# Performance work log

Measured on AMD Instinct MI355X. Metric: run time of the kernel, lower is better.

Reference implementation:

```python
import jax, jax.numpy as jnp
import numpy as np
import math

B, S, D, H = 2, 2048, 2048, 16
HD = D // H  # head_dim = 128
NEG = -9e15


def setup_inputs() -> dict:
    key = jax.random.key(0)
    k1, k2, k3 = jax.random.split(key, 3)
    x = jax.random.normal(k1, (B, S, D), dtype=jnp.float32)
    Wqkv = jax.random.normal(k2, (D, 3 * D), dtype=jnp.float32) * (1.0 / math.sqrt(D))
    bqkv = jnp.zeros((3 * D,), dtype=jnp.float32)
    Wo = jax.random.normal(k3, (D, D), dtype=jnp.float32) * (1.0 / math.sqrt(D))
    bo = jnp.zeros((D,), dtype=jnp.float32)
    return {"x": x, "Wqkv": Wqkv, "bqkv": bqkv, "Wo": Wo, "bo": bo}


def reference(x, Wqkv, bqkv, Wo, bo):
    b, s, d = x.shape
    # fused QKV projection
    qkv = x @ Wqkv + bqkv                       # [B,S,3D]
    qkv = qkv.reshape(b, s, H, 3 * HD)          # per-head interleaved q|k|v
    qkv = qkv.transpose(0, 2, 1, 3)             # [B,H,S,3*HD]
    q, k, v = jnp.split(qkv, 3, axis=-1)        # each [B,H,S,HD]
    scale = 1.0 / math.sqrt(HD)
    logits = jnp.einsum('bhqd,bhkd->bhqk', q, k) * scale  # [B,H,S,S]
    causal = jnp.tril(jnp.ones((s, s), dtype=bool))[None, None]
    logits = jnp.where(causal, logits, NEG)
    score = jax.nn.softmax(logits, axis=-1)
    attn = jnp.einsum('bhqk,bhkd->bhqd', score, v)         # [B,H,S,HD]
    attn = attn.transpose(0, 2, 1, 3).reshape(b, s, d)
    return attn @ Wo + bo
```

## Files before the change

kernel.cpp:

```cpp
#include <hip/hip_runtime.h>
#include <stdint.h>

#define DEV static __device__ __forceinline__

typedef _Float16 half8 __attribute__((ext_vector_type(8)));
typedef float f32x4 __attribute__((ext_vector_type(4)));

constexpr int Bc = 2, Sc = 2048, Dc = 2048, Hc = 16, HDc = 128;
constexpr int D3c = 3 * Dc;
constexpr int Mc = Bc * Sc;

DEV void gl_lds16(const void* g, void* l) {
    __builtin_amdgcn_global_load_lds(
        (const __attribute__((address_space(1))) unsigned int*)g,
        (__attribute__((address_space(3))) unsigned int*)l,
        16, 0, 0);
}

__global__ __launch_bounds__(256) void cast_f16_kernel(
    const float* __restrict__ in, _Float16* __restrict__ out)
{
    int i = blockIdx.x * 256 + threadIdx.x;
    const float4* p = (const float4*)in;
    float4 a = p[i * 2], b = p[i * 2 + 1];
    half8 hv;
    hv[0] = (_Float16)a.x; hv[1] = (_Float16)a.y; hv[2] = (_Float16)a.z; hv[3] = (_Float16)a.w;
    hv[4] = (_Float16)b.x; hv[5] = (_Float16)b.y; hv[6] = (_Float16)b.z; hv[7] = (_Float16)b.w;
    *(half8*)(out + (size_t)i * 8) = hv;
}

__global__ __launch_bounds__(256) void transpose_cast_kernel(
    const float* __restrict__ in, _Float16* __restrict__ out, int R, int C)
{
    __shared__ float ls[64][65];
    const int t = threadIdx.x;
    const int r0 = blockIdx.y * 64, c0 = blockIdx.x * 64;
    const int rr = t >> 6, cc = t & 63;
#pragma unroll
    for (int i = 0; i < 16; ++i) {
        int r = i * 4 + rr;
        ls[r][cc] = in[(size_t)(r0 + r) * C + c0 + cc];
    }
    __syncthreads();
#pragma unroll
    for (int i = 0; i < 16; ++i) {
        int r = i * 4 + rr;
        out[(size_t)(c0 + r) * R + r0 + cc] = (_Float16)ls[cc][r];
    }
}

__global__ __launch_bounds__(256) void transpose_v_kernel(
    const uint16_t* __restrict__ qkv, uint16_t* __restrict__ vt)
{
    __shared__ uint32_t ls[64][65];
    const int t = threadIdx.x;
    const int s0 = blockIdx.x * 64, d0 = blockIdx.y * 64, bh = blockIdx.z;
    const int b = bh >> 4, h = bh & 15;
    const int rr = t >> 6, cc = t & 63;
#pragma unroll
    for (int i = 0; i < 16; ++i) {
        int r = i * 4 + rr;
        ls[r][cc] = qkv[(size_t)(b * Sc + s0 + r) * D3c + h * 384 + 256 + d0 + cc];
    }
    __syncthreads();
#pragma unroll
    for (int i = 0; i < 16; ++i) {
        int r = i * 4 + rr;
        vt[(size_t)(bh * HDc + d0 + r) * Sc + s0 + cc] = (uint16_t)ls[cc][r];
    }
}

template <int BF16OUT>
__global__ __launch_bounds__(256, 2) void gemm_bt_kernel(
    const _Float16* __restrict__ A, const _Float16* __restrict__ Bt,
    const float* __restrict__ bias, void* __restrict__ Cout,
    int M, int N, int K)
{
    __shared__ __align__(16) char smem[32768];
    char* sA = smem;
    char* sB = smem + 16384;
    const int t = threadIdx.x, w = t >> 6, lane = t & 63;
    const int quad = lane >> 4, l15 = lane & 15;
    const int wr = w >> 1, wc = w & 1;
    const int n0 = blockIdx.x * 128, m0 = blockIdx.y * 128;

    const f32x4 vzero = {0.f, 0.f, 0.f, 0.f};
    f32x4 acc[4][4];
#pragma unroll
    for (int i = 0; i < 4; ++i)
#pragma unroll
        for (int j = 0; j < 4; ++j) acc[i][j] = vzero;

    const int kiters = K >> 6;
    for (int kk = 0; kk < kiters; ++kk) {
#pragma unroll
        for (int i = 0; i < 4; ++i) {
            int c = i * 256 + t;
            int row = c >> 3, kbs = c & 7, kact = kbs ^ (row & 7);
            gl_lds16(A + (size_t)(m0 + row) * K + kk * 64 + kact * 8,
                     sA + (i * 256 + w * 64) * 16);
        }
#pragma unroll
        for (int i = 0; i < 4; ++i) {
            int c = i * 256 + t;
            int row = c >> 3, kbs = c & 7, kact = kbs ^ (row & 7);
            gl_lds16(Bt + (size_t)(n0 + row) * K + kk * 64 + kact * 8,
                     sB + (i * 256 + w * 64) * 16);
        }
        __syncthreads();
#pragma unroll
        for (int ks = 0; ks < 2; ++ks) {
            half8 af[4], bf[4];
#pragma unroll
            for (int mt = 0; mt < 4; ++mt) {
                int row = wr * 64 + mt * 16 + l15;
                int kact = (ks * 4 + quad) ^ (l15 & 7);
                af[mt] = *(const half8*)(sA + row * 128 + kact * 16);
            }
#pragma unroll
            for (int nt = 0; nt < 4; ++nt) {
                int row = wc * 64 + nt * 16 + l15;
                int kact = (ks * 4 + quad) ^ (l15 & 7);
                bf[nt] = *(const half8*)(sB + row * 128 + kact * 16);
            }
#pragma unroll
            for (int mt = 0; mt < 4; ++mt)
#pragma unroll
                for (int nt = 0; nt < 4; ++nt)
                    acc[mt][nt] = __builtin_amdgcn_mfma_f32_16x16x32_f16(
                        af[mt], bf[nt], acc[mt][nt], 0, 0, 0);
        }
        __syncthreads();
    }

#pragma unroll
    for (int nt = 0; nt < 4; ++nt) {
        int col = n0 + wc * 64 + nt * 16 + l15;
        float bv = bias[col];
#pragma unroll
        for (int mt = 0; mt < 4; ++mt)
#pragma unroll
            for (int r = 0; r < 4; ++r) {
                int row = m0 + wr * 64 + mt * 16 + quad * 4 + r;
                float v = acc[mt][nt][r] + bv;
                if (BF16OUT) ((_Float16*)Cout)[(size_t)row * N + col] = (_Float16)v;
                else         ((float*)Cout)[(size_t)row * N + col] = v;
            }
    }
}

__global__ __launch_bounds__(256, 2) void flash_kernel(
    const _Float16* __restrict__ qkv, const _Float16* __restrict__ vt,
    _Float16* __restrict__ attn)
{
    __shared__ __align__(16) char smem[49152];
    char* sK = smem;
    char* sV = smem + 16384;
    char* sP = smem + 32768;

    const int t = threadIdx.x, w = t >> 6, lane = t & 63;
    const int quad = lane >> 4, l15 = lane & 15;
    const int qt = 15 - blockIdx.x;
    const int bh = blockIdx.y;
    const int b = bh >> 4, h = bh & 15;
    const int q0 = qt * 128;

    half8 qf[2][4];
#pragma unroll
    for (int mt = 0; mt < 2; ++mt)
#pragma unroll
        for (int ks = 0; ks < 4; ++ks) {
            const _Float16* p = qkv +
                (size_t)(b * Sc + q0 + w * 32 + mt * 16 + l15) * D3c +
                h * 384 + ks * 32 + quad * 8;
            qf[mt][ks] = *(const half8*)p;
        }

    const f32x4 vzero = {0.f, 0.f, 0.f, 0.f};
    f32x4 o[2][8];
#pragma unroll
    for (int mt = 0; mt < 2; ++mt)
#pragma unroll
        for (int dt = 0; dt < 8; ++dt) o[mt][dt] = vzero;
    float m_st[2][4], l_st[2][4];
#pragma unroll
    for (int mt = 0; mt < 2; ++mt)
#pragma unroll
        for (int r = 0; r < 4; ++r) { m_st[mt][r] = -1e30f; l_st[mt][r] = 0.f; }

    const float kScale = 0.08838834764831845f * 1.4426950408889634f;
    const int nkt = 2 * qt + 2;

    for (int kt = 0; kt < nkt; ++kt) {
#pragma unroll
        for (int i = 0; i < 4; ++i) {
            int c = i * 256 + t;
            int row = c >> 4, kbs = c & 15, kact = kbs ^ (row & 15);
            gl_lds16(qkv + (size_t)(b * Sc + kt * 64 + row) * D3c + h * 384 + 128 + kact * 8,
                     sK + (i * 256 + w * 64) * 16);
        }
#pragma unroll
        for (int i = 0; i < 4; ++i) {
            int c = i * 256 + t;
            int row = c >> 3, kbs = c & 7, kact = kbs ^ (row & 7);
            gl_lds16(vt + (size_t)(bh * HDc + row) * Sc + kt * 64 + kact * 8,
                     sV + (i * 256 + w * 64) * 16);
        }
        __syncthreads();

        f32x4 sf[2][4];
#pragma unroll
        for (int mt = 0; mt < 2; ++mt)
#pragma unroll
            for (int nt = 0; nt < 4; ++nt) sf[mt][nt] = vzero;
#pragma unroll
        for (int ks = 0; ks < 4; ++ks) {
            half8 bk[4];
#pragma unroll
            for (int nt = 0; nt < 4; ++nt) {
                int row = nt * 16 + l15;
                int kact = (ks * 4 + quad) ^ l15;
                bk[nt] = *(const half8*)(sK + row * 256 + kact * 16);
            }
#pragma unroll
            for (int mt = 0; mt < 2; ++mt)
#pragma unroll
                for (int nt = 0; nt < 4; ++nt)
                    sf[mt][nt] = __builtin_amdgcn_mfma_f32_16x16x32_f16(
                        qf[mt][ks], bk[nt], sf[mt][nt], 0, 0, 0);
        }

        const bool domask = (kt >= 2 * qt);
        float rm[2][4];
#pragma unroll
        for (int mt = 0; mt < 2; ++mt)
#pragma unroll
            for (int r = 0; r < 4; ++r) rm[mt][r] = -1e30f;
#pragma unroll
        for (int mt = 0; mt < 2; ++mt)
#pragma unroll
            for (int nt = 0; nt < 4; ++nt)
#pragma unroll
                for (int r = 0; r < 4; ++r) {
                    float v = sf[mt][nt][r] * kScale;
                    if (domask) {
                        int col = kt * 64 + nt * 16 + l15;
                        int rowq = q0 + w * 32 + mt * 16 + quad * 4 + r;
                        if (col > rowq) v = -1e30f;
                    }
                    sf[mt][nt][r] = v;
                    rm[mt][r] = fmaxf(rm[mt][r], v);
                }
#pragma unroll
        for (int mt = 0; mt < 2; ++mt)
#pragma unroll
            for (int r = 0; r < 4; ++r) {
                float v = rm[mt][r];
                v = fmaxf(v, __shfl_xor(v, 1, 16));
                v = fmaxf(v, __shfl_xor(v, 2, 16));
                v = fmaxf(v, __shfl_xor(v, 4, 16));
                v = fmaxf(v, __shfl_xor(v, 8, 16));
                rm[mt][r] = v;
            }
        float alpha[2][4], rs[2][4];
#pragma unroll
        for (int mt = 0; mt < 2; ++mt)
#pragma unroll
            for (int r = 0; r < 4; ++r) {
                float mn = fmaxf(m_st[mt][r], rm[mt][r]);
                alpha[mt][r] = __builtin_amdgcn_exp2f(m_st[mt][r] - mn);
                m_st[mt][r] = mn;
                rs[mt][r] = 0.f;
            }
#pragma unroll
        for (int mt = 0; mt < 2; ++mt)
#pragma unroll
            for (int nt = 0; nt < 4; ++nt)
#pragma unroll
                for (int r = 0; r < 4; ++r) {
                    float p = __builtin_amdgcn_exp2f(sf[mt][nt][r] - m_st[mt][r]);
                    rs[mt][r] += p;
                    int row = w * 32 + mt * 16 + quad * 4 + r;
                    int col = nt * 16 + l15;
                    int chunk = (col >> 3) ^ (row & 7);
                    *(_Float16*)(sP + row * 128 + chunk * 16 + (col & 7) * 2) = (_Float16)p;
                }
#pragma unroll
        for (int mt = 0; mt < 2; ++mt)
#pragma unroll
            for (int r = 0; r < 4; ++r) {
                float v = rs[mt][r];
                v += __shfl_xor(v, 1, 16);
                v += __shfl_xor(v, 2, 16);
                v += __shfl_xor(v, 4, 16);
                v += __shfl_xor(v, 8, 16);
                l_st[mt][r] = l_st[mt][r] * alpha[mt][r] + v;
            }
#pragma unroll
        for (int mt = 0; mt < 2; ++mt)
#pragma unroll
            for (int dt = 0; dt < 8; ++dt)
#pragma unroll
                for (int r = 0; r < 4; ++r) o[mt][dt][r] *= alpha[mt][r];
        __syncthreads();

#pragma unroll
        for (int kk = 0; kk < 2; ++kk) {
            int chunk = (kk * 4 + quad) ^ (l15 & 7);
            half8 ap[2], bv[8];
#pragma unroll
            for (int mt = 0; mt < 2; ++mt) {
                int row = w * 32 + mt * 16 + l15;
                ap[mt] = *(const half8*)(sP + row * 128 + chunk * 16);
            }
#pragma unroll
            for (int dt = 0; dt < 8; ++dt) {
                int row = dt * 16 + l15;
                bv[dt] = *(const half8*)(sV + row * 128 + chunk * 16);
            }
#pragma unroll
            for (int mt = 0; mt < 2; ++mt)
#pragma unroll
                for (int dt = 0; dt < 8; ++dt)
                    o[mt][dt] = __builtin_amdgcn_mfma_f32_16x16x32_f16(
                        ap[mt], bv[dt], o[mt][dt], 0, 0, 0);
        }
        __syncthreads();
    }

#pragma unroll
    for (int mt = 0; mt < 2; ++mt) {
        float linv[4];
#pragma unroll
        for (int r = 0; r < 4; ++r) linv[r] = 1.0f / l_st[mt][r];
#pragma unroll
        for (int dt = 0; dt < 8; ++dt)
#pragma unroll
            for (int r = 0; r < 4; ++r) {
                int row = q0 + w * 32 + mt * 16 + quad * 4 + r;
                int col = h * HDc + dt * 16 + l15;
                attn[(size_t)(b * Sc + row) * Dc + col] = (_Float16)(o[mt][dt][r] * linv[r]);
            }
    }
}

extern "C" void kernel_launch(void* const* d_in, const int* in_sizes, int n_in,
                              void* d_out, int out_size, void* d_ws, size_t ws_size,
                              hipStream_t stream)
{
    (void)in_sizes; (void)n_in; (void)out_size; (void)ws_size;
    const float* x    = (const float*)d_in[0];
    const float* Wqkv = (const float*)d_in[1];
    const float* bqkv = (const float*)d_in[2];
    const float* Wo   = (const float*)d_in[3];
    const float* bo   = (const float*)d_in[4];
    float* out = (float*)d_out;

    _Float16* xb  = (_Float16*)d_ws;
    _Float16* wt1 = xb  + (size_t)Mc * Dc;
    _Float16* wt2 = wt1 + (size_t)D3c * Dc;
    _Float16* qkv = wt2 + (size_t)Dc * Dc;
    _Float16* vtg  = wt1;
    _Float16* attn = xb;

    cast_f16_kernel<<<Mc * Dc / 2048, 256, 0, stream>>>(x, xb);
    transpose_cast_kernel<<<dim3(D3c / 64, Dc / 64), 256, 0, stream>>>(Wqkv, wt1, Dc, D3c);
    transpose_cast_kernel<<<dim3(Dc / 64, Dc / 64), 256, 0, stream>>>(Wo, wt2, Dc, Dc);
    gemm_bt_kernel<1><<<dim3(D3c / 128, Mc / 128), 256, 0, stream>>>(
        xb, wt1, bqkv, qkv, Mc, D3c, Dc);
    transpose_v_kernel<<<dim3(Sc / 64, 2, Bc * Hc), 256, 0, stream>>>(
        (const uint16_t*)qkv, (uint16_t*)vtg);
    flash_kernel<<<dim3(16, Bc * Hc), 256, 0, stream>>>(qkv, vtg, attn);
    gemm_bt_kernel<0><<<dim3(Dc / 128, Mc / 128), 256, 0, stream>>>(
        attn, wt2, bo, out, Mc, Dc, Dc);
}
```

Measured before the change: 438.6 us.

## Restructure flash attention to keep P in registers via transposed S tiles

The flash kernel now computes S^T (K as the A operand, Q as the B operand), so each lane holds one query row's probabilities. It converts these to half4 and feeds them straight into 16x16x16 MFMAs against V, which removes the LDS round-trip for P and one barrier per tile. The query tile shrinks from 128 to 64 rows, LDS drops to 32KB, and launch bounds rise to 4 blocks per CU. The grid is reordered so heads vary fastest, and the output is staged through LDS for coalesced 16-byte stores. The trade-offs are a smaller MFMA shape with more K/V reloads per query, in exchange for higher occupancy and finer causal load balancing.

```diff
diff --git a/kernel.cpp b/kernel.cpp
--- a/kernel.cpp
+++ b/kernel.cpp
@@ -4,6 +4,7 @@
 #define DEV static __device__ __forceinline__
 
 typedef _Float16 half8 __attribute__((ext_vector_type(8)));
+typedef _Float16 half4 __attribute__((ext_vector_type(4)));
 typedef float f32x4 __attribute__((ext_vector_type(4)));
 
 constexpr int Bc = 2, Sc = 2048, Dc = 2048, Hc = 16, HDc = 128;
@@ -149,47 +150,38 @@
     }
 }
 
-__global__ __launch_bounds__(256, 2) void flash_kernel(
+__global__ __launch_bounds__(256, 4) void flash_kernel(
     const _Float16* __restrict__ qkv, const _Float16* __restrict__ vt,
     _Float16* __restrict__ attn)
 {
-    __shared__ __align__(16) char smem[49152];
+    __shared__ __align__(16) char smem[32768];
     char* sK = smem;
     char* sV = smem + 16384;
-    char* sP = smem + 32768;
 
     const int t = threadIdx.x, w = t >> 6, lane = t & 63;
     const int quad = lane >> 4, l15 = lane & 15;
-    const int qt = 15 - blockIdx.x;
-    const int bh = blockIdx.y;
+    const int bh = blockIdx.x;
+    const int qt = 31 - blockIdx.y;
     const int b = bh >> 4, h = bh & 15;
-    const int q0 = qt * 128;
-
-    half8 qf[2][4];
-#pragma unroll
-    for (int mt = 0; mt < 2; ++mt)
-#pragma unroll
-        for (int ks = 0; ks < 4; ++ks) {
-            const _Float16* p = qkv +
-                (size_t)(b * Sc + q0 + w * 32 + mt * 16 + l15) * D3c +
-                h * 384 + ks * 32 + quad * 8;
-            qf[mt][ks] = *(const half8*)p;
-        }
+    const int q0 = qt * 64;
+    const int qrow = q0 + w * 16 + l15;
+
+    half8 qf[4];
+#pragma unroll
+    for (int ks = 0; ks < 4; ++ks) {
+        const _Float16* p = qkv + (size_t)(b * Sc + qrow) * D3c +
+                            h * 384 + ks * 32 + quad * 8;
+        qf[ks] = *(const half8*)p;
+    }
 
     const f32x4 vzero = {0.f, 0.f, 0.f, 0.f};
-    f32x4 o[2][8];
-#pragma unroll
-    for (int mt = 0; mt < 2; ++mt)
-#pragma unroll
-        for (int dt = 0; dt < 8; ++dt) o[mt][dt] = vzero;
-    float m_st[2][4], l_st[2][4];
-#pragma unroll
-    for (int mt = 0; mt < 2; ++mt)
-#pragma unroll
-        for (int r = 0; r < 4; ++r) { m_st[mt][r] = -1e30f; l_st[mt][r] = 0.f; }
+    f32x4 o[8];
+#pragma unroll
+    for (int dt = 0; dt < 8; ++dt) o[dt] = vzero;
+    float m_st = -1e30f, l_st = 0.f;
 
     const float kScale = 0.08838834764831845f * 1.4426950408889634f;
-    const int nkt = 2 * qt + 2;
+    const int nkt = qt + 1;
 
     for (int kt = 0; kt < nkt; ++kt) {
 #pragma unroll
@@ -208,139 +200,88 @@
         }
         __syncthreads();
 
-        f32x4 sf[2][4];
-#pragma unroll
-        for (int mt = 0; mt < 2; ++mt)
-#pragma unroll
-            for (int nt = 0; nt < 4; ++nt) sf[mt][nt] = vzero;
+        f32x4 sf[4];
+#pragma unroll
+        for (int kb = 0; kb < 4; ++kb) sf[kb] = vzero;
 #pragma unroll
         for (int ks = 0; ks < 4; ++ks) {
-            half8 bk[4];
-#pragma unroll
-            for (int nt = 0; nt < 4; ++nt) {
-                int row = nt * 16 + l15;
-                int kact = (ks * 4 + quad) ^ l15;
-                bk[nt] = *(const half8*)(sK + row * 256 + kact * 16);
-            }
-#pragma unroll
-            for (int mt = 0; mt < 2; ++mt)
-#pragma unroll
-                for (int nt = 0; nt < 4; ++nt)
-                    sf[mt][nt] = __builtin_amdgcn_mfma_f32_16x16x32_f16(
-                        qf[mt][ks], bk[nt], sf[mt][nt], 0, 0, 0);
-        }
-
-        const bool domask = (kt >= 2 * qt);
-        float rm[2][4];
-#pragma unroll
-        for (int mt = 0; mt < 2; ++mt)
-#pragma unroll
-            for (int r = 0; r < 4; ++r) rm[mt][r] = -1e30f;
-#pragma unroll
-        for (int mt = 0; mt < 2; ++mt)
-#pragma unroll
-            for (int nt = 0; nt < 4; ++nt)
-#pragma unroll
-                for (int r = 0; r < 4; ++r) {
-                    float v = sf[mt][nt][r] * kScale;
-                    if (domask) {
-                        int col = kt * 64 + nt * 16 + l15;
-                        int rowq = q0 + w * 32 + mt * 16 + quad * 4 + r;
-                        if (col > rowq) v = -1e30f;
-                    }
-                    sf[mt][nt][r] = v;
-                    rm[mt][r] = fmaxf(rm[mt][r], v);
+#pragma unroll
+            for (int kb = 0; kb < 4; ++kb) {
+                int row = kb * 16 + l15;
+                int slot = (ks * 4 + quad) ^ l15;
+                half8 kf = *(const half8*)(sK + row * 256 + slot * 16);
+                sf[kb] = __builtin_amdgcn_mfma_f32_16x16x32_f16(kf, qf[ks], sf[kb], 0, 0, 0);
+            }
+        }
+
+        const bool domask = (kt == qt);
+        float rm = -1e30f;
+#pragma unroll
+        for (int kb = 0; kb < 4; ++kb)
+#pragma unroll
+            for (int r = 0; r < 4; ++r) {
+                float v = sf[kb][r] * kScale;
+                if (domask) {
+                    int col = kt * 64 + kb * 16 + quad * 4 + r;
+                    if (col > qrow) v = -1e30f;
                 }
-#pragma unroll
-        for (int mt = 0; mt < 2; ++mt)
+                sf[kb][r] = v;
+                rm = fmaxf(rm, v);
+            }
+        rm = fmaxf(rm, __shfl_xor(rm, 16, 64));
+        rm = fmaxf(rm, __shfl_xor(rm, 32, 64));
+        float mn = fmaxf(m_st, rm);
+        float alpha = __builtin_amdgcn_exp2f(m_st - mn);
+        m_st = mn;
+
+        half4 pb[4];
+        float rs = 0.f;
+#pragma unroll
+        for (int kb = 0; kb < 4; ++kb)
 #pragma unroll
             for (int r = 0; r < 4; ++r) {
-                float v = rm[mt][r];
-                v = fmaxf(v, __shfl_xor(v, 1, 16));
-                v = fmaxf(v, __shfl_xor(v, 2, 16));
-                v = fmaxf(v, __shfl_xor(v, 4, 16));
-                v = fmaxf(v, __shfl_xor(v, 8, 16));
-                rm[mt][r] = v;
-            }
-        float alpha[2][4], rs[2][4];
-#pragma unroll
-        for (int mt = 0; mt < 2; ++mt)
-#pragma unroll
-            for (int r = 0; r < 4; ++r) {
-                float mn = fmaxf(m_st[mt][r], rm[mt][r]);
-                alpha[mt][r] = __builtin_amdgcn_exp2f(m_st[mt][r] - mn);
-                m_st[mt][r] = mn;
-                rs[mt][r] = 0.f;
-            }
-#pragma unroll
-        for (int mt = 0; mt < 2; ++mt)
-#pragma unroll
-            for (int nt = 0; nt < 4; ++nt)
-#pragma unroll
-                for (int r = 0; r < 4; ++r) {
-                    float p = __builtin_amdgcn_exp2f(sf[mt][nt][r] - m_st[mt][r]);
-                    rs[mt][r] += p;
-                    int row = w * 32 + mt * 16 + quad * 4 + r;
-                    int col = nt * 16 + l15;
-                    int chunk = (col >> 3) ^ (row & 7);
-                    *(_Float16*)(sP + row * 128 + chunk * 16 + (col & 7) * 2) = (_Float16)p;
-                }
-#pragma unroll
-        for (int mt = 0; mt < 2; ++mt)
-#pragma unroll
-            for (int r = 0; r < 4; ++r) {
-                float v = rs[mt][r];
-                v += __shfl_xor(v, 1, 16);
-                v += __shfl_xor(v, 2, 16);
-                v += __shfl_xor(v, 4, 16);
-                v += __shfl_xor(v, 8, 16);
-                l_st[mt][r] = l_st[mt][r] * alpha[mt][r] + v;
-            }
-#pragma unroll
-        for (int mt = 0; mt < 2; ++mt)
-#pragma unroll
-            for (int dt = 0; dt < 8; ++dt)
-#pragma unroll
-                for (int r = 0; r < 4; ++r) o[mt][dt][r] *= alpha[mt][r];
-        __syncthreads();
-
-#pragma unroll
-        for (int kk = 0; kk < 2; ++kk) {
-            int chunk = (kk * 4 + quad) ^ (l15 & 7);
-            half8 ap[2], bv[8];
-#pragma unroll
-            for (int mt = 0; mt < 2; ++mt) {
-                int row = w * 32 + mt * 16 + l15;
-                ap[mt] = *(const half8*)(sP + row * 128 + chunk * 16);
-            }
+                float p = __builtin_amdgcn_exp2f(sf[kb][r] - mn);
+                rs += p;
+                pb[kb][r] = (_Float16)p;
+            }
+        rs += __shfl_xor(rs, 16, 64);
+        rs += __shfl_xor(rs, 32, 64);
+        l_st = l_st * alpha + rs;
+
+#pragma unroll
+        for (int dt = 0; dt < 8; ++dt)
+#pragma unroll
+            for (int r = 0; r < 4; ++r) o[dt][r] *= alpha;
+
+#pragma unroll
+        for (int kb = 0; kb < 4; ++kb) {
 #pragma unroll
             for (int dt = 0; dt < 8; ++dt) {
                 int row = dt * 16 + l15;
-                bv[dt] = *(const half8*)(sV + row * 128 + chunk * 16);
-            }
-#pragma unroll
-            for (int mt = 0; mt < 2; ++mt)
-#pragma unroll
-                for (int dt = 0; dt < 8; ++dt)
-                    o[mt][dt] = __builtin_amdgcn_mfma_f32_16x16x32_f16(
-                        ap[mt], bv[dt], o[mt][dt], 0, 0, 0);
+                int slot = (kb * 2 + (quad >> 1)) ^ (l15 & 7);
+                half4 vf = *(const half4*)(sV + row * 128 + slot * 16 + (quad & 1) * 8);
+                o[dt] = __builtin_amdgcn_mfma_f32_16x16x16f16(vf, pb[kb], o[dt], 0, 0, 0);
+            }
         }
         __syncthreads();
     }
 
-#pragma unroll
-    for (int mt = 0; mt < 2; ++mt) {
-        float linv[4];
-#pragma unroll
-        for (int r = 0; r < 4; ++r) linv[r] = 1.0f / l_st[mt][r];
-#pragma unroll
-        for (int dt = 0; dt < 8; ++dt)
-#pragma unroll
-            for (int r = 0; r < 4; ++r) {
-                int row = q0 + w * 32 + mt * 16 + quad * 4 + r;
-                int col = h * HDc + dt * 16 + l15;
-                attn[(size_t)(b * Sc + row) * Dc + col] = (_Float16)(o[mt][dt][r] * linv[r]);
-            }
+    char* sO = smem;
+    float linv = 1.0f / l_st;
+#pragma unroll
+    for (int dt = 0; dt < 8; ++dt) {
+        half4 hv;
+#pragma unroll
+        for (int r = 0; r < 4; ++r) hv[r] = (_Float16)(o[dt][r] * linv);
+        *(half4*)(sO + (w * 16 + l15) * 272 + (dt * 16 + quad * 4) * 2) = hv;
+    }
+    __syncthreads();
+#pragma unroll
+    for (int i = 0; i < 4; ++i) {
+        int q = i * 16 + (t >> 4);
+        int d = (t & 15) * 8;
+        half8 hv = *(const half8*)(sO + q * 272 + d * 2);
+        *(half8*)(attn + (size_t)(b * Sc + q0 + q) * Dc + h * HDc + d) = hv;
     }
 }
 
@@ -370,7 +311,7 @@
         xb, wt1, bqkv, qkv, Mc, D3c, Dc);
     transpose_v_kernel<<<dim3(Sc / 64, 2, Bc * Hc), 256, 0, stream>>>(
         (const uint16_t*)qkv, (uint16_t*)vtg);
-    flash_kernel<<<dim3(16, Bc * Hc), 256, 0, stream>>>(qkv, vtg, attn);
+    flash_kernel<<<dim3(Bc * Hc, 32), 256, 0, stream>>>(qkv, vtg, attn);
     gemm_bt_kernel<0><<<dim3(Dc / 128, Mc / 128), 256, 0, stream>>>(
         attn, wt2, bo, out, Mc, Dc, Dc);
 }
```

Result: faster. 392.3 us (-10.6%).
